# Optimization experiments

Measured on AMD Instinct MI355X. Metric: run time of the kernel, lower is better.

## Reference

```python
import jax, jax.numpy as jnp
import numpy as np
import math


def setup_inputs() -> dict:
    key = jax.random.key(0)
    ks = jax.random.split(key, 6)
    B, L, D, H, R = 4, 2048, 512, 8, 4  # batch, seq, feature_dim, n_heads, n_hashes
    hd = D // H
    x = jax.random.normal(ks[0], (B, L, D), jnp.float32)
    Wqk = jax.random.normal(ks[1], (D, 2 * D), jnp.float32) * 0.02
    bqk = jnp.zeros((2 * D,), jnp.float32)
    Wv = jax.random.normal(ks[2], (D, D), jnp.float32) * 0.02
    bv = jnp.zeros((D,), jnp.float32)
    Wo = jax.random.normal(ks[3], (D, D), jnp.float32) * 0.02
    bo = jnp.zeros((D,), jnp.float32)
    rotations = jax.random.normal(ks[4], (H, R, hd), jnp.float32) * 0.02  # registered buffer
    return {"x": x, "Wqk": Wqk, "bqk": bqk, "Wv": Wv, "bv": bv,
            "Wo": Wo, "bo": bo, "rotations": rotations}


def reference(x, Wqk, bqk, Wv, bv, Wo, bo, rotations):
    B, L, D = x.shape
    H = rotations.shape[0]
    hd = D // H

    qk = x @ Wqk + bqk                      # [B, L, 2D]
    q, k = jnp.split(qk, 2, axis=-1)
    v = x @ Wv + bv                         # [B, L, D]

    def heads(t):  # [B, L, D] -> [B, H, L, hd]
        return t.reshape(B, L, H, hd).transpose(0, 2, 1, 3)

    q, k, v = heads(q), heads(k), heads(v)

    # LSH hashing of Q: random rotations then argmax over [rot, -rot]
    rotated = jnp.einsum('bhld,hrd->bhlr', q, rotations)           # [B, H, L, R]
    buckets = jnp.argmax(jnp.concatenate([rotated, -rotated], axis=-1), axis=-1)  # [B, H, L]

    # bucket-sort gather along sequence
    idx = jnp.argsort(buckets, axis=-1)                            # [B, H, L]
    gather = lambda t: jnp.take_along_axis(t, idx[..., None], axis=2)
    sq, sk, sv = gather(q), gather(k), gather(v)

    # full attention over the bucket-sorted sequence (as in the source)
    dots = jnp.einsum('bhid,bhjd->bhij', sq, sk) / math.sqrt(hd)   # [B, H, L, L]
    attn = jax.nn.softmax(dots, axis=-1)
    out = jnp.einsum('bhij,bhjd->bhid', attn, sv)                  # [B, H, L, hd]

    # restore original sequence order
    restore = jnp.argsort(idx, axis=-1)
    out = jnp.take_along_axis(out, restore[..., None], axis=2)
    out = out.transpose(0, 2, 1, 3).reshape(B, L, D)
    return out @ Wo + bo
```

## Files before the change

kernel.cpp:

```cpp
#include <hip/hip_runtime.h>
#include <hip/hip_bf16.h>
#include <hip/hip_fp16.h>
#include <math.h>


typedef __attribute__((ext_vector_type(8))) short bf16x8;
typedef __attribute__((ext_vector_type(4))) float f32x4;

#define LOG2E_8 0.1803368801111244f

__device__ __forceinline__ ushort f2bf(float f) {
    union { float f; uint u; } v; v.f = f;
    uint r = v.u + 0x7fffu + ((v.u >> 16) & 1u);
    return (ushort)(r >> 16);
}

__device__ __forceinline__ uint pk2bf(float a, float b) {
    union { __hip_bfloat162 h; uint u; } c;
    c.h = __float22bfloat162_rn(make_float2(a, b));
    return c.u;
}

__device__ __forceinline__ float fast_exp2(float x) {
#if __has_builtin(__builtin_amdgcn_exp2f)
    return __builtin_amdgcn_exp2f(x);
#else
    return exp2f(x);
#endif
}

__device__ __forceinline__ void gload16(const ushort* g, ushort* l) {
    __builtin_amdgcn_global_load_lds(
        (const __attribute__((address_space(1))) uint*)(g),
        (__attribute__((address_space(3))) uint*)(l), 16, 0, 0);
}

__global__ __launch_bounds__(256) void prep_all(
    const float* __restrict__ x, const float* __restrict__ Wqk,
    const float* __restrict__ Wv, const float* __restrict__ Wo,
    const float* __restrict__ bqk, const float* __restrict__ bv,
    ushort* __restrict__ xb, ushort* __restrict__ Wt,
    ushort* __restrict__ Wot, float* __restrict__ biasqkv)
{
    int t = blockIdx.x * 256 + threadIdx.x;
    const int NX = 8192 * 512 / 4, N1 = 512 * 1024, N2 = 512 * 512;
    if (t < NX) {
        float4 v = ((const float4*)x)[t];
        ushort4 o; o.x = f2bf(v.x); o.y = f2bf(v.y); o.z = f2bf(v.z); o.w = f2bf(v.w);
        ((ushort4*)xb)[t] = o;
    } else if (t < NX + N1) {
        int u = t - NX; int k = u >> 10, n = u & 1023;
        Wt[(size_t)n * 512 + k] = f2bf(Wqk[u]);
    } else if (t < NX + N1 + N2) {
        int u = t - NX - N1; int k = u >> 9, n = u & 511;
        Wt[(size_t)(1024 + n) * 512 + k] = f2bf(Wv[u]);
    } else if (t < NX + N1 + 2 * N2) {
        int u = t - NX - N1 - N2; int k = u >> 9, n = u & 511;
        Wot[(size_t)n * 512 + k] = f2bf(Wo[u]);
    } else if (t < NX + N1 + 2 * N2 + 1536) {
        int u = t - NX - N1 - 2 * N2;
        biasqkv[u] = (u < 1024) ? bqk[u] : bv[u - 1024];
    }
}

__global__ __launch_bounds__(256) void mfma_gemm_qkv(
    const ushort* __restrict__ A, const ushort* __restrict__ Bt,
    const float* __restrict__ bias,
    ushort* __restrict__ qkout, ushort* __restrict__ vtout)
{
    __shared__ ushort SA[8192];
    __shared__ ushort SB[8192];

    const int tid = threadIdx.x, lane = tid & 63, wave = tid >> 6;
    const int quad = lane >> 4, l16 = lane & 15;
    const int m0 = blockIdx.y * 128, n0 = blockIdx.x * 128;
    const int sub = lane >> 3, gl = lane & 7;
    const int wm = (wave >> 1) * 64, wn = (wave & 1) * 64;

    const ushort* asrc[4]; const ushort* bsrc[4];
    #pragma unroll
    for (int n = 0; n < 4; ++n) {
        int row = wave * 32 + n * 8 + sub;
        int g = gl ^ (row & 7);
        asrc[n] = A  + (size_t)(m0 + row) * 512 + g * 8;
        bsrc[n] = Bt + (size_t)(n0 + row) * 512 + g * 8;
    }

    f32x4 acc[4][4];
    #pragma unroll
    for (int mi = 0; mi < 4; ++mi)
        #pragma unroll
        for (int nj = 0; nj < 4; ++nj) acc[mi][nj] = (f32x4){0.f, 0.f, 0.f, 0.f};

    for (int k0 = 0; k0 < 512; k0 += 64) {
        __syncthreads();
        #pragma unroll
        for (int n = 0; n < 4; ++n) {
            gload16(asrc[n] + k0, &SA[(wave * 32 + n * 8) * 64]);
            gload16(bsrc[n] + k0, &SB[(wave * 32 + n * 8) * 64]);
        }
        __syncthreads();

        #pragma unroll
        for (int kc = 0; kc < 2; ++kc) {
            bf16x8 af[4], bfr[4];
            #pragma unroll
            for (int mi = 0; mi < 4; ++mi) {
                int row = wm + mi * 16 + l16;
                af[mi] = *(const bf16x8*)&SA[row * 64 + (((kc * 4 + quad) ^ (row & 7)) * 8)];
            }
            #pragma unroll
            for (int nj = 0; nj < 4; ++nj) {
                int row = wn + nj * 16 + l16;
                bfr[nj] = *(const bf16x8*)&SB[row * 64 + (((kc * 4 + quad) ^ (row & 7)) * 8)];
            }
            #pragma unroll
            for (int mi = 0; mi < 4; ++mi)
                #pragma unroll
                for (int nj = 0; nj < 4; ++nj)
                    acc[mi][nj] = __builtin_amdgcn_mfma_f32_16x16x32_bf16(
                        af[mi], bfr[nj], acc[mi][nj], 0, 0, 0);
        }
    }

    float bvv[4];
    #pragma unroll
    for (int nj = 0; nj < 4; ++nj) bvv[nj] = bias[n0 + wn + nj * 16 + l16];

    if (n0 < 1024) {
        const float sc = (n0 < 512) ? LOG2E_8 : 1.0f;
        #pragma unroll
        for (int mi = 0; mi < 4; ++mi)
            #pragma unroll
            for (int nj = 0; nj < 4; ++nj)
                #pragma unroll
                for (int r = 0; r < 4; ++r) {
                    size_t row = m0 + wm + mi * 16 + quad * 4 + r;
                    qkout[row * 1024 + n0 + wn + nj * 16 + l16] =
                        f2bf((acc[mi][nj][r] + bvv[nj]) * sc);
                }
    } else {
        const int bb = m0 >> 11;
        #pragma unroll
        for (int mi = 0; mi < 4; ++mi)
            #pragma unroll
            for (int nj = 0; nj < 4; ++nj) {
                int nv = n0 - 1024 + wn + nj * 16 + l16;
                int hh = nv >> 6, d = nv & 63;
                int lpos = (m0 & 2047) + wm + (mi >> 1) * 32 + (mi & 1) * 4 + quad * 8;
                uint2 st;
                st.x = pk2bf(acc[mi][nj][0] + bvv[nj], acc[mi][nj][1] + bvv[nj]);
                st.y = pk2bf(acc[mi][nj][2] + bvv[nj], acc[mi][nj][3] + bvv[nj]);
                *(uint2*)&vtout[((size_t)(bb * 8 + hh) * 64 + d) * 2048 + lpos] = st;
            }
    }
}

__global__ __launch_bounds__(256) void attn_mfma(
    const ushort* __restrict__ qk, const ushort* __restrict__ vt,
    __half* __restrict__ Opart, float* __restrict__ Lpart)
{
    __shared__ ushort LDSU[16384];

    const int tid = threadIdx.x, lane = tid & 63, wave = tid >> 6;
    const int quad = lane >> 4, l16 = lane & 15;
    const int bh = blockIdx.x, b = bh >> 3, h = bh & 7;
    const int qblk = blockIdx.y, s = blockIdx.z;
    const int q0 = qblk * 128 + wave * 32;
    const int blin = (bh * 16 + qblk) * 2 + s;
    const int sub = lane >> 3, gl = lane & 7;

    bf16x8 qf[2][2];
    #pragma unroll
    for (int g = 0; g < 2; ++g)
        #pragma unroll
        for (int kc = 0; kc < 2; ++kc)
            qf[g][kc] = *(const bf16x8*)&qk[(size_t)(b * 2048 + q0 + g * 16 + l16) * 1024
                                           + h * 64 + kc * 32 + quad * 8];

    const int kb0 = l16 * 64 + ((quad ^ (l16 & 7)) << 3);
    const int kb1 = l16 * 64 + (((4 | quad) ^ (l16 & 7)) << 3);

    const int srow = wave * 16 + sub;
    const int g0 = gl ^ (srow & 7), g1 = gl ^ ((srow + 8) & 7);
    const ushort* k0p = qk + (size_t)(b * 2048 + s * 1024 + srow)     * 1024 + 512 + h * 64 + g0 * 8;
    const ushort* k1p = qk + (size_t)(b * 2048 + s * 1024 + srow + 8) * 1024 + 512 + h * 64 + g1 * 8;
    const ushort* v0p = vt + ((size_t)bh * 64 + srow)     * 2048 + s * 1024 + g0 * 8;
    const ushort* v1p = vt + ((size_t)bh * 64 + srow + 8) * 2048 + s * 1024 + g1 * 8;

    f32x4 O[2][4];
    #pragma unroll
    for (int g = 0; g < 2; ++g)
        #pragma unroll
        for (int nd = 0; nd < 4; ++nd) O[g][nd] = (f32x4){0.f, 0.f, 0.f, 0.f};
    float lsum[2] = {0.f, 0.f};

    gload16(k0p, &LDSU[wave * 1024]);
    gload16(k1p, &LDSU[wave * 1024 + 512]);
    gload16(v0p, &LDSU[8192 + wave * 1024]);
    gload16(v1p, &LDSU[8192 + wave * 1024 + 512]);
    k0p += 65536; k1p += 65536; v0p += 64; v1p += 64;
    __syncthreads();

#define ATILE(B)                                                               \
    {                                                                          \
        gload16(k0p, &LDSU[((B) ^ 1) * 4096 + wave * 1024]);                   \
        gload16(k1p, &LDSU[((B) ^ 1) * 4096 + wave * 1024 + 512]);             \
        gload16(v0p, &LDSU[8192 + ((B) ^ 1) * 4096 + wave * 1024]);            \
        gload16(v1p, &LDSU[8192 + ((B) ^ 1) * 4096 + wave * 1024 + 512]);      \
        k0p += 65536; k1p += 65536; v0p += 64; v1p += 64;                      \
        f32x4 S[2][4];                                                         \
        _Pragma("unroll")                                                      \
        for (int g = 0; g < 2; ++g)                                            \
            _Pragma("unroll")                                                  \
            for (int mik = 0; mik < 4; ++mik)                                  \
                S[g][mik] = (f32x4){0.f, 0.f, 0.f, 0.f};                       \
        _Pragma("unroll")                                                      \
        for (int mik = 0; mik < 4; ++mik) {                                    \
            bf16x8 kf0 = *(const bf16x8*)&LDSU[(B) * 4096 + mik * 1024 + kb0]; \
            bf16x8 kf1 = *(const bf16x8*)&LDSU[(B) * 4096 + mik * 1024 + kb1]; \
            S[0][mik] = __builtin_amdgcn_mfma_f32_16x16x32_bf16(kf0, qf[0][0], S[0][mik], 0, 0, 0); \
            S[1][mik] = __builtin_amdgcn_mfma_f32_16x16x32_bf16(kf0, qf[1][0], S[1][mik], 0, 0, 0); \
            S[0][mik] = __builtin_amdgcn_mfma_f32_16x16x32_bf16(kf1, qf[0][1], S[0][mik], 0, 0, 0); \
            S[1][mik] = __builtin_amdgcn_mfma_f32_16x16x32_bf16(kf1, qf[1][1], S[1][mik], 0, 0, 0); \
        }                                                                      \
        uint pkk[2][4][2];                                                     \
        _Pragma("unroll")                                                      \
        for (int g = 0; g < 2; ++g) {                                          \
            float part = 0.f;                                                  \
            _Pragma("unroll")                                                  \
            for (int mik = 0; mik < 4; ++mik) {                                \
                _Pragma("unroll")                                              \
                for (int r = 0; r < 4; ++r) {                                  \
                    float e = fast_exp2(S[g][mik][r]);                         \
                    S[g][mik][r] = e;                                          \
                    part += e;                                                 \
                }                                                              \
                pkk[g][mik][0] = pk2bf(S[g][mik][0], S[g][mik][1]);            \
                pkk[g][mik][1] = pk2bf(S[g][mik][2], S[g][mik][3]);            \
            }                                                                  \
            part += __shfl_xor(part, 16);                                      \
            part += __shfl_xor(part, 32);                                      \
            lsum[g] += part;                                                   \
        }                                                                      \
        _Pragma("unroll")                                                      \
        for (int c = 0; c < 2; ++c) {                                          \
            union { uint u[4]; bf16x8 v; } a0, a1;                             \
            a0.u[0] = pkk[0][2 * c][0]; a0.u[1] = pkk[0][2 * c][1];            \
            a0.u[2] = pkk[0][2 * c + 1][0]; a0.u[3] = pkk[0][2 * c + 1][1];    \
            a1.u[0] = pkk[1][2 * c][0]; a1.u[1] = pkk[1][2 * c][1];            \
            a1.u[2] = pkk[1][2 * c + 1][0]; a1.u[3] = pkk[1][2 * c + 1][1];    \
            _Pragma("unroll")                                                  \
            for (int nd = 0; nd < 4; ++nd) {                                   \
                bf16x8 vb = *(const bf16x8*)&LDSU[8192 + (B) * 4096 + nd * 1024 + ((c) ? kb1 : kb0)]; \
                O[0][nd] = __builtin_amdgcn_mfma_f32_16x16x32_bf16(a0.v, vb, O[0][nd], 0, 0, 0); \
                O[1][nd] = __builtin_amdgcn_mfma_f32_16x16x32_bf16(a1.v, vb, O[1][nd], 0, 0, 0); \
            }                                                                  \
        }                                                                      \
        __syncthreads();                                                       \
    }

    for (int t2 = 0; t2 < 8; ++t2) {
        ATILE(0);
        ATILE(1);
    }
#undef ATILE

    #pragma unroll
    for (int g = 0; g < 2; ++g) {
        if (quad == 0)
            Lpart[(size_t)blin * 128 + wave * 32 + g * 16 + l16] = lsum[g];
        #pragma unroll
        for (int nd = 0; nd < 4; ++nd)
            #pragma unroll
            for (int r = 0; r < 4; ++r)
                Opart[(size_t)blin * 8192 + (wave * 32 + g * 16 + quad * 4 + r) * 64
                      + nd * 16 + l16] = __float2half(O[g][nd][r]);
    }
}

__global__ __launch_bounds__(256) void combine(
    const __half* __restrict__ Opart, const float* __restrict__ Lpart,
    ushort* __restrict__ attnb)
{
    int gidx = blockIdx.x * 256 + threadIdx.x;
    int rid = gidx >> 2, l = gidx & 3;
    int bh = rid >> 11, rem = rid & 2047;
    int pb = (bh * 16 + (rem >> 7)) * 2;
    int q = rem & 127;

    float inv = 1.f / (Lpart[(size_t)pb * 128 + q] + Lpart[(size_t)(pb + 1) * 128 + q]);

    size_t o0 = (size_t)pb * 8192 + q * 64 + l * 16;
    union { uint4 v; __half2 h[4]; } r0a, r0b, r1a, r1b;
    r0a.v = *(const uint4*)(Opart + o0);
    r0b.v = *(const uint4*)(Opart + o0 + 8);
    r1a.v = *(const uint4*)(Opart + o0 + 8192);
    r1b.v = *(const uint4*)(Opart + o0 + 8192 + 8);

    union { ushort u[8]; uint4 v; } st[2];
    #pragma unroll
    for (int i = 0; i < 4; ++i) {
        float2 a = __half22float2(r0a.h[i]), c = __half22float2(r1a.h[i]);
        st[0].u[i * 2]     = f2bf((a.x + c.x) * inv);
        st[0].u[i * 2 + 1] = f2bf((a.y + c.y) * inv);
        float2 e = __half22float2(r0b.h[i]), f = __half22float2(r1b.h[i]);
        st[1].u[i * 2]     = f2bf((e.x + f.x) * inv);
        st[1].u[i * 2 + 1] = f2bf((e.y + f.y) * inv);
    }
    size_t orow = (size_t)(bh >> 3) * 2048 + rem;
    *(uint4*)&attnb[orow * 512 + (bh & 7) * 64 + l * 16]     = st[0].v;
    *(uint4*)&attnb[orow * 512 + (bh & 7) * 64 + l * 16 + 8] = st[1].v;
}

__global__ __launch_bounds__(256) void mfma_gemm_out(
    const ushort* __restrict__ A, const ushort* __restrict__ Bt,
    const float* __restrict__ bias, float* __restrict__ Cf)
{
    __shared__ ushort SA[8192];
    __shared__ ushort SB[4096];

    const int tid = threadIdx.x, lane = tid & 63, wave = tid >> 6;
    const int quad = lane >> 4, l16 = lane & 15;
    const int m0 = blockIdx.y * 128, n0 = blockIdx.x * 64;
    const int sub = lane >> 3, gl = lane & 7;

    const ushort* asrc[4]; const ushort* bsrc[2];
    #pragma unroll
    for (int n = 0; n < 4; ++n) {
        int row = wave * 32 + n * 8 + sub;
        int g = gl ^ (row & 7);
        asrc[n] = A + (size_t)(m0 + row) * 512 + g * 8;
    }
    #pragma unroll
    for (int n = 0; n < 2; ++n) {
        int row = wave * 16 + n * 8 + sub;
        int g = gl ^ (row & 7);
        bsrc[n] = Bt + (size_t)(n0 + row) * 512 + g * 8;
    }

    f32x4 acc[2][4];
    #pragma unroll
    for (int mi = 0; mi < 2; ++mi)
        #pragma unroll
        for (int nj = 0; nj < 4; ++nj) acc[mi][nj] = (f32x4){0.f, 0.f, 0.f, 0.f};

    for (int k0 = 0; k0 < 512; k0 += 64) {
        __syncthreads();
        #pragma unroll
        for (int n = 0; n < 4; ++n)
            gload16(asrc[n] + k0, &SA[(wave * 32 + n * 8) * 64]);
        #pragma unroll
        for (int n = 0; n < 2; ++n)
            gload16(bsrc[n] + k0, &SB[(wave * 16 + n * 8) * 64]);
        __syncthreads();

        #pragma unroll
        for (int kc = 0; kc < 2; ++kc) {
            bf16x8 af[2], bfr[4];
            #pragma unroll
            for (int mi = 0; mi < 2; ++mi) {
                int row = wave * 32 + mi * 16 + l16;
                af[mi] = *(const bf16x8*)&SA[row * 64 + (((kc * 4 + quad) ^ (row & 7)) * 8)];
            }
            #pragma unroll
            for (int nj = 0; nj < 4; ++nj) {
                int row = nj * 16 + l16;
                bfr[nj] = *(const bf16x8*)&SB[row * 64 + (((kc * 4 + quad) ^ (row & 7)) * 8)];
            }
            #pragma unroll
            for (int mi = 0; mi < 2; ++mi)
                #pragma unroll
                for (int nj = 0; nj < 4; ++nj)
                    acc[mi][nj] = __builtin_amdgcn_mfma_f32_16x16x32_bf16(
                        af[mi], bfr[nj], acc[mi][nj], 0, 0, 0);
        }
    }

    float bvv[4];
    #pragma unroll
    for (int nj = 0; nj < 4; ++nj) bvv[nj] = bias[n0 + nj * 16 + l16];

    #pragma unroll
    for (int mi = 0; mi < 2; ++mi)
        #pragma unroll
        for (int nj = 0; nj < 4; ++nj)
            #pragma unroll
            for (int r = 0; r < 4; ++r) {
                size_t row = m0 + wave * 32 + mi * 16 + quad * 4 + r;
                Cf[row * 512 + n0 + nj * 16 + l16] = acc[mi][nj][r] + bvv[nj];
            }
}

extern "C" void kernel_launch(void* const* d_in, const int* in_sizes, int n_in,
                              void* d_out, int out_size, void* d_ws, size_t ws_size,
                              hipStream_t stream)
{
    const float* x   = (const float*)d_in[0];
    const float* Wqk = (const float*)d_in[1];
    const float* bqk = (const float*)d_in[2];
    const float* Wv  = (const float*)d_in[3];
    const float* bv  = (const float*)d_in[4];
    const float* Wo  = (const float*)d_in[5];
    const float* bo  = (const float*)d_in[6];
    float* out = (float*)d_out;

    ushort* xb    = (ushort*)d_ws;
    ushort* qkb   = xb + (size_t)8192 * 512;
    ushort* vtb   = qkb + (size_t)8192 * 1024;
    ushort* attnb = vtb + (size_t)32 * 64 * 2048;
    ushort* Wt    = attnb + (size_t)8192 * 512;
    ushort* Wot   = Wt + (size_t)1536 * 512;
    float* biasqkv = (float*)(Wot + (size_t)512 * 512);
    __half* Opart = (__half*)(biasqkv + 2048);
    float*  Lpart = (float*)(Opart + (size_t)1024 * 8192);

    prep_all<<<8199, 256, 0, stream>>>(x, Wqk, Wv, Wo, bqk, bv, xb, Wt, Wot, biasqkv);

    mfma_gemm_qkv<<<dim3(12, 64), 256, 0, stream>>>(xb, Wt, biasqkv, qkb, vtb);

    attn_mfma<<<dim3(32, 16, 2), 256, 0, stream>>>(qkb, vtb, Opart, Lpart);
    combine<<<1024, 256, 0, stream>>>(Opart, Lpart, attnb);

    mfma_gemm_out<<<dim3(8, 64), 256, 0, stream>>>(attnb, Wot, bo, out);
}
```

Baseline: 174.6 us.

## Fuse split-K attention halves into one block and drop combine kernel

Each attention block now runs 512 threads: two wave groups each handle half of the key range, and their partial outputs and row sums are merged through LDS in-kernel. This removes the separate combine kernel and the fp16 partial-output round trip through global memory. The row sums are now computed with an MFMA against a ones vector instead of shuffle reductions, exp uses inline v_exp_f32, and bf16 packing switches from round-to-nearest to truncation via perm. The costs are more LDS per block and a barrier before the merge, plus a small precision change from the truncated bf16 probabilities.

```diff
diff --git a/kernel.cpp b/kernel.cpp
--- a/kernel.cpp
+++ b/kernel.cpp
@@ -1,6 +1,5 @@
 #include <hip/hip_runtime.h>
 #include <hip/hip_bf16.h>
-#include <hip/hip_fp16.h>
 #include <math.h>
 
 
@@ -21,12 +20,18 @@
     return c.u;
 }
 
-__device__ __forceinline__ float fast_exp2(float x) {
-#if __has_builtin(__builtin_amdgcn_exp2f)
-    return __builtin_amdgcn_exp2f(x);
-#else
-    return exp2f(x);
-#endif
+__device__ __forceinline__ float vexp2(float x) {
+    float r;
+    asm volatile("v_exp_f32 %0, %1\n\ts_nop 0" : "=v"(r) : "v"(x));
+    return r;
+}
+
+__device__ __forceinline__ uint f2u(float x) {
+    union { float f; uint u; } c; c.f = x; return c.u;
+}
+
+__device__ __forceinline__ uint pktrunc(float hi, float lo) {
+    return __builtin_amdgcn_perm(f2u(hi), f2u(lo), 0x07060302u);
 }
 
 __device__ __forceinline__ void gload16(const ushort* g, ushort* l) {
@@ -156,19 +161,20 @@
     }
 }
 
-__global__ __launch_bounds__(256) void attn_mfma(
+__global__ __launch_bounds__(512, 4) void attn_mfma(
     const ushort* __restrict__ qk, const ushort* __restrict__ vt,
-    __half* __restrict__ Opart, float* __restrict__ Lpart)
+    ushort* __restrict__ aout)
 {
-    __shared__ ushort LDSU[16384];
+    __shared__ ushort LDSU[32768];
 
     const int tid = threadIdx.x, lane = tid & 63, wave = tid >> 6;
     const int quad = lane >> 4, l16 = lane & 15;
+    const int grp = wave >> 2, w4 = wave & 3;
     const int bh = blockIdx.x, b = bh >> 3, h = bh & 7;
-    const int qblk = blockIdx.y, s = blockIdx.z;
-    const int q0 = qblk * 128 + wave * 32;
-    const int blin = (bh * 16 + qblk) * 2 + s;
+    const int qblk = blockIdx.y;
+    const int q0 = qblk * 128 + w4 * 32;
     const int sub = lane >> 3, gl = lane & 7;
+    const int GK = grp * 16384, GV = GK + 8192;
 
     bf16x8 qf[2][2];
     #pragma unroll
@@ -178,36 +184,41 @@
             qf[g][kc] = *(const bf16x8*)&qk[(size_t)(b * 2048 + q0 + g * 16 + l16) * 1024
                                            + h * 64 + kc * 32 + quad * 8];
 
-    const int kb0 = l16 * 64 + ((quad ^ (l16 & 7)) << 3);
-    const int kb1 = l16 * 64 + (((4 | quad) ^ (l16 & 7)) << 3);
-
-    const int srow = wave * 16 + sub;
+    bf16x8 ONES;
+    #pragma unroll
+    for (int i = 0; i < 8; ++i) ONES[i] = (short)0x3F80;
+
+    const int r0 = l16 * 64 + ((quad ^ (l16 & 7)) << 3);
+    const int r1 = l16 * 64 + (((4 | quad) ^ (l16 & 7)) << 3);
+
+    const int srow = w4 * 16 + sub;
     const int g0 = gl ^ (srow & 7), g1 = gl ^ ((srow + 8) & 7);
-    const ushort* k0p = qk + (size_t)(b * 2048 + s * 1024 + srow)     * 1024 + 512 + h * 64 + g0 * 8;
-    const ushort* k1p = qk + (size_t)(b * 2048 + s * 1024 + srow + 8) * 1024 + 512 + h * 64 + g1 * 8;
-    const ushort* v0p = vt + ((size_t)bh * 64 + srow)     * 2048 + s * 1024 + g0 * 8;
-    const ushort* v1p = vt + ((size_t)bh * 64 + srow + 8) * 2048 + s * 1024 + g1 * 8;
-
-    f32x4 O[2][4];
-    #pragma unroll
-    for (int g = 0; g < 2; ++g)
+    const ushort* k0p = qk + (size_t)(b * 2048 + grp * 1024 + srow)     * 1024 + 512 + h * 64 + g0 * 8;
+    const ushort* k1p = qk + (size_t)(b * 2048 + grp * 1024 + srow + 8) * 1024 + 512 + h * 64 + g1 * 8;
+    const ushort* v0p = vt + ((size_t)bh * 64 + srow)     * 2048 + grp * 1024 + g0 * 8;
+    const ushort* v1p = vt + ((size_t)bh * 64 + srow + 8) * 2048 + grp * 1024 + g1 * 8;
+
+    f32x4 O[2][4], Lacc[2];
+    #pragma unroll
+    for (int g = 0; g < 2; ++g) {
+        Lacc[g] = (f32x4){0.f, 0.f, 0.f, 0.f};
         #pragma unroll
         for (int nd = 0; nd < 4; ++nd) O[g][nd] = (f32x4){0.f, 0.f, 0.f, 0.f};
-    float lsum[2] = {0.f, 0.f};
-
-    gload16(k0p, &LDSU[wave * 1024]);
-    gload16(k1p, &LDSU[wave * 1024 + 512]);
-    gload16(v0p, &LDSU[8192 + wave * 1024]);
-    gload16(v1p, &LDSU[8192 + wave * 1024 + 512]);
+    }
+
+    gload16(k0p, &LDSU[GK + w4 * 1024]);
+    gload16(k1p, &LDSU[GK + w4 * 1024 + 512]);
+    gload16(v0p, &LDSU[GV + w4 * 1024]);
+    gload16(v1p, &LDSU[GV + w4 * 1024 + 512]);
     k0p += 65536; k1p += 65536; v0p += 64; v1p += 64;
     __syncthreads();
 
 #define ATILE(B)                                                               \
     {                                                                          \
-        gload16(k0p, &LDSU[((B) ^ 1) * 4096 + wave * 1024]);                   \
-        gload16(k1p, &LDSU[((B) ^ 1) * 4096 + wave * 1024 + 512]);             \
-        gload16(v0p, &LDSU[8192 + ((B) ^ 1) * 4096 + wave * 1024]);            \
-        gload16(v1p, &LDSU[8192 + ((B) ^ 1) * 4096 + wave * 1024 + 512]);      \
+        gload16(k0p, &LDSU[GK + ((B) ^ 1) * 4096 + w4 * 1024]);                \
+        gload16(k1p, &LDSU[GK + ((B) ^ 1) * 4096 + w4 * 1024 + 512]);          \
+        gload16(v0p, &LDSU[GV + ((B) ^ 1) * 4096 + w4 * 1024]);                \
+        gload16(v1p, &LDSU[GV + ((B) ^ 1) * 4096 + w4 * 1024 + 512]);          \
         k0p += 65536; k1p += 65536; v0p += 64; v1p += 64;                      \
         f32x4 S[2][4];                                                         \
         _Pragma("unroll")                                                      \
@@ -217,8 +228,8 @@
                 S[g][mik] = (f32x4){0.f, 0.f, 0.f, 0.f};                       \
         _Pragma("unroll")                                                      \
         for (int mik = 0; mik < 4; ++mik) {                                    \
-            bf16x8 kf0 = *(const bf16x8*)&LDSU[(B) * 4096 + mik * 1024 + kb0]; \
-            bf16x8 kf1 = *(const bf16x8*)&LDSU[(B) * 4096 + mik * 1024 + kb1]; \
+            bf16x8 kf0 = *(const bf16x8*)&LDSU[GK + (B) * 4096 + mik * 1024 + r0]; \
+            bf16x8 kf1 = *(const bf16x8*)&LDSU[GK + (B) * 4096 + mik * 1024 + r1]; \
             S[0][mik] = __builtin_amdgcn_mfma_f32_16x16x32_bf16(kf0, qf[0][0], S[0][mik], 0, 0, 0); \
             S[1][mik] = __builtin_amdgcn_mfma_f32_16x16x32_bf16(kf0, qf[1][0], S[1][mik], 0, 0, 0); \
             S[0][mik] = __builtin_amdgcn_mfma_f32_16x16x32_bf16(kf1, qf[0][1], S[0][mik], 0, 0, 0); \
@@ -226,23 +237,15 @@
         }                                                                      \
         uint pkk[2][4][2];                                                     \
         _Pragma("unroll")                                                      \
-        for (int g = 0; g < 2; ++g) {                                          \
-            float part = 0.f;                                                  \
+        for (int g = 0; g < 2; ++g)                                            \
             _Pragma("unroll")                                                  \
             for (int mik = 0; mik < 4; ++mik) {                                \
                 _Pragma("unroll")                                              \
-                for (int r = 0; r < 4; ++r) {                                  \
-                    float e = fast_exp2(S[g][mik][r]);                         \
-                    S[g][mik][r] = e;                                          \
-                    part += e;                                                 \
-                }                                                              \
-                pkk[g][mik][0] = pk2bf(S[g][mik][0], S[g][mik][1]);            \
-                pkk[g][mik][1] = pk2bf(S[g][mik][2], S[g][mik][3]);            \
+                for (int r = 0; r < 4; ++r)                                    \
+                    S[g][mik][r] = vexp2(S[g][mik][r]);                        \
+                pkk[g][mik][0] = pktrunc(S[g][mik][1], S[g][mik][0]);          \
+                pkk[g][mik][1] = pktrunc(S[g][mik][3], S[g][mik][2]);          \
             }                                                                  \
-            part += __shfl_xor(part, 16);                                      \
-            part += __shfl_xor(part, 32);                                      \
-            lsum[g] += part;                                                   \
-        }                                                                      \
         _Pragma("unroll")                                                      \
         for (int c = 0; c < 2; ++c) {                                          \
             union { uint u[4]; bf16x8 v; } a0, a1;                             \
@@ -250,9 +253,11 @@
             a0.u[2] = pkk[0][2 * c + 1][0]; a0.u[3] = pkk[0][2 * c + 1][1];    \
             a1.u[0] = pkk[1][2 * c][0]; a1.u[1] = pkk[1][2 * c][1];            \
             a1.u[2] = pkk[1][2 * c + 1][0]; a1.u[3] = pkk[1][2 * c + 1][1];    \
+            Lacc[0] = __builtin_amdgcn_mfma_f32_16x16x32_bf16(a0.v, ONES, Lacc[0], 0, 0, 0); \
+            Lacc[1] = __builtin_amdgcn_mfma_f32_16x16x32_bf16(a1.v, ONES, Lacc[1], 0, 0, 0); \
             _Pragma("unroll")                                                  \
             for (int nd = 0; nd < 4; ++nd) {                                   \
-                bf16x8 vb = *(const bf16x8*)&LDSU[8192 + (B) * 4096 + nd * 1024 + ((c) ? kb1 : kb0)]; \
+                bf16x8 vb = *(const bf16x8*)&LDSU[GV + (B) * 4096 + nd * 1024 + ((c) ? r1 : r0)]; \
                 O[0][nd] = __builtin_amdgcn_mfma_f32_16x16x32_bf16(a0.v, vb, O[0][nd], 0, 0, 0); \
                 O[1][nd] = __builtin_amdgcn_mfma_f32_16x16x32_bf16(a1.v, vb, O[1][nd], 0, 0, 0); \
             }                                                                  \
@@ -266,51 +271,42 @@
     }
 #undef ATILE
 
-    #pragma unroll
-    for (int g = 0; g < 2; ++g) {
-        if (quad == 0)
-            Lpart[(size_t)blin * 128 + wave * 32 + g * 16 + l16] = lsum[g];
-        #pragma unroll
-        for (int nd = 0; nd < 4; ++nd)
+    float* XO = (float*)&LDSU[16384];
+    float* XL = (float*)&LDSU[0];
+
+    if (grp == 1) {
+        #pragma unroll
+        for (int g = 0; g < 2; ++g) {
+            if (l16 == 0)
+                #pragma unroll
+                for (int r = 0; r < 4; ++r)
+                    XL[w4 * 32 + g * 16 + quad * 4 + r] = Lacc[g][r];
+            #pragma unroll
+            for (int nd = 0; nd < 4; ++nd)
+                #pragma unroll
+                for (int r = 0; r < 4; ++r)
+                    XO[(w4 * 32 + g * 16 + quad * 4 + r) * 64 + nd * 16 + l16] = O[g][nd][r];
+        }
+    }
+    __syncthreads();
+    if (grp == 0) {
+        #pragma unroll
+        for (int g = 0; g < 2; ++g) {
+            float inv[4];
             #pragma unroll
             for (int r = 0; r < 4; ++r)
-                Opart[(size_t)blin * 8192 + (wave * 32 + g * 16 + quad * 4 + r) * 64
-                      + nd * 16 + l16] = __float2half(O[g][nd][r]);
-    }
-}
-
-__global__ __launch_bounds__(256) void combine(
-    const __half* __restrict__ Opart, const float* __restrict__ Lpart,
-    ushort* __restrict__ attnb)
-{
-    int gidx = blockIdx.x * 256 + threadIdx.x;
-    int rid = gidx >> 2, l = gidx & 3;
-    int bh = rid >> 11, rem = rid & 2047;
-    int pb = (bh * 16 + (rem >> 7)) * 2;
-    int q = rem & 127;
-
-    float inv = 1.f / (Lpart[(size_t)pb * 128 + q] + Lpart[(size_t)(pb + 1) * 128 + q]);
-
-    size_t o0 = (size_t)pb * 8192 + q * 64 + l * 16;
-    union { uint4 v; __half2 h[4]; } r0a, r0b, r1a, r1b;
-    r0a.v = *(const uint4*)(Opart + o0);
-    r0b.v = *(const uint4*)(Opart + o0 + 8);
-    r1a.v = *(const uint4*)(Opart + o0 + 8192);
-    r1b.v = *(const uint4*)(Opart + o0 + 8192 + 8);
-
-    union { ushort u[8]; uint4 v; } st[2];
-    #pragma unroll
-    for (int i = 0; i < 4; ++i) {
-        float2 a = __half22float2(r0a.h[i]), c = __half22float2(r1a.h[i]);
-        st[0].u[i * 2]     = f2bf((a.x + c.x) * inv);
-        st[0].u[i * 2 + 1] = f2bf((a.y + c.y) * inv);
-        float2 e = __half22float2(r0b.h[i]), f = __half22float2(r1b.h[i]);
-        st[1].u[i * 2]     = f2bf((e.x + f.x) * inv);
-        st[1].u[i * 2 + 1] = f2bf((e.y + f.y) * inv);
-    }
-    size_t orow = (size_t)(bh >> 3) * 2048 + rem;
-    *(uint4*)&attnb[orow * 512 + (bh & 7) * 64 + l * 16]     = st[0].v;
-    *(uint4*)&attnb[orow * 512 + (bh & 7) * 64 + l * 16 + 8] = st[1].v;
+                inv[r] = 1.f / (Lacc[g][r] + XL[w4 * 32 + g * 16 + quad * 4 + r]);
+            #pragma unroll
+            for (int nd = 0; nd < 4; ++nd)
+                #pragma unroll
+                for (int r = 0; r < 4; ++r) {
+                    float o1 = XO[(w4 * 32 + g * 16 + quad * 4 + r) * 64 + nd * 16 + l16];
+                    size_t row = (size_t)b * 2048 + q0 + g * 16 + quad * 4 + r;
+                    aout[row * 512 + h * 64 + nd * 16 + l16] =
+                        f2bf((O[g][nd][r] + o1) * inv[r]);
+                }
+        }
+    }
 }
 
 __global__ __launch_bounds__(256) void mfma_gemm_out(
@@ -412,15 +408,12 @@
     ushort* Wt    = attnb + (size_t)8192 * 512;
     ushort* Wot   = Wt + (size_t)1536 * 512;
     float* biasqkv = (float*)(Wot + (size_t)512 * 512);
-    __half* Opart = (__half*)(biasqkv + 2048);
-    float*  Lpart = (float*)(Opart + (size_t)1024 * 8192);
 
     prep_all<<<8199, 256, 0, stream>>>(x, Wqk, Wv, Wo, bqk, bv, xb, Wt, Wot, biasqkv);
 
     mfma_gemm_qkv<<<dim3(12, 64), 256, 0, stream>>>(xb, Wt, biasqkv, qkb, vtb);
 
-    attn_mfma<<<dim3(32, 16, 2), 256, 0, stream>>>(qkb, vtb, Opart, Lpart);
-    combine<<<1024, 256, 0, stream>>>(Opart, Lpart, attnb);
+    attn_mfma<<<dim3(32, 16), 512, 0, stream>>>(qkb, vtb, attnb);
 
     mfma_gemm_out<<<dim3(8, 64), 256, 0, stream>>>(attnb, Wot, bo, out);
 }
```

Result: faster. 157.5 us (-9.8%).
